# Performance work log

Hardware: AMD Instinct MI355X
Metric: run time of the kernel (lower is better)

The kernel has to match this reference:

```python
import jax, jax.numpy as jnp
import numpy as np

V, D, S, H, L, BATCH = 32000, 1024, 1024, 16, 8, 2
HD = D // H  # head_size = 64


def _pyramid_mask(block_size):
    # Faithful to the torch buffer construction of 'pyr' for BIDIRECTIONAL mode.
    h = block_size // 2
    tril = np.tril(np.ones((h, h), dtype=np.float32))
    top = np.repeat(np.flip(tril, axis=1), 2, axis=0)            # (block_size, h)
    reps = np.array([2] * (h - 1) + [1])
    bot = np.concatenate([np.zeros((1, h), dtype=np.float32),
                          np.repeat(tril, reps, axis=0)], axis=0)  # (block_size, h)
    return np.concatenate([top, bot], axis=1)                     # (block_size, block_size)


def _layernorm(x, g, b, eps=1e-5):
    mu = jnp.mean(x, axis=-1, keepdims=True)
    var = jnp.mean((x - mu) ** 2, axis=-1, keepdims=True)
    return (x - mu) * jax.lax.rsqrt(var + eps) * g + b


def setup_inputs() -> dict:
    key = jax.random.key(0)
    ks = jax.random.split(key, 12)
    sd = 0.02
    inp = {
        "idx": jax.random.randint(ks[0], (BATCH, S), 0, V),
        "tok_emb": jax.random.normal(ks[1], (V, D), jnp.float32) * sd,
        "pos_emb": jax.random.normal(ks[2], (S, D), jnp.float32) * sd,
        "ln1_g": jnp.ones((L, D), jnp.float32),
        "ln1_b": jnp.zeros((L, D), jnp.float32),
        "wq": jax.random.normal(ks[3], (L, D, D), jnp.float32) * sd,
        "wk": jax.random.normal(ks[4], (L, D, D), jnp.float32) * sd,
        "wv": jax.random.normal(ks[5], (L, D, D), jnp.float32) * sd,
        "wproj": jax.random.normal(ks[6], (L, D, D), jnp.float32) * sd,
        "bproj": jnp.zeros((L, D), jnp.float32),
        "ln2_g": jnp.ones((L, D), jnp.float32),
        "ln2_b": jnp.zeros((L, D), jnp.float32),
        "w1": jax.random.normal(ks[7], (L, D, 4 * D), jnp.float32) * sd,
        "b1": jnp.zeros((L, 4 * D), jnp.float32),
        "w2": jax.random.normal(ks[8], (L, 4 * D, D), jnp.float32) * sd,
        "b2": jnp.zeros((L, D), jnp.float32),
        "lnf_g": jnp.ones((D,), jnp.float32),
        "lnf_b": jnp.zeros((D,), jnp.float32),
        "wlm": jax.random.normal(ks[9], (D, 2 * V), jnp.float32) * sd,
        "blm": jnp.zeros((2 * V,), jnp.float32),
    }
    return inp


def reference(idx, tok_emb, pos_emb, ln1_g, ln1_b, wq, wk, wv, wproj, bproj,
              ln2_g, ln2_b, w1, b1, w2, b2, lnf_g, lnf_b, wlm, blm):
    B, T = idx.shape
    # pyr[:T, (S-T)//2 : S - (S-T)//2]; with T == S this is the full mask.
    pyr = jnp.asarray(_pyramid_mask(S))
    lo = (S - T) // 2
    mask = pyr[:T, lo:S - lo] == 0  # True where masked out
    scale = HD ** -0.5

    x = tok_emb[idx] + pos_emb[:T]  # [B, T, D]
    for l in range(L):
        h = _layernorm(x, ln1_g[l], ln1_b[l])
        q = (h @ wq[l]).reshape(B, T, H, HD)
        k = (h @ wk[l]).reshape(B, T, H, HD)
        v = (h @ wv[l]).reshape(B, T, H, HD)
        wei = jnp.einsum('bthd,bshd->bhts', q, k) * scale  # [B, H, T, T]
        wei = jnp.where(mask, -jnp.inf, wei)
        wei = jax.nn.softmax(wei, axis=-1)  # dropout=0 (eval)
        att = jnp.einsum('bhts,bshd->bthd', wei, v).reshape(B, T, D)
        x = x + att @ wproj[l] + bproj[l]
        h2 = _layernorm(x, ln2_g[l], ln2_b[l])
        x = x + jax.nn.relu(h2 @ w1[l] + b1[l]) @ w2[l] + b2[l]
    x = _layernorm(x, lnf_g, lnf_b)
    logits = x @ wlm + blm  # [B, T, 2*V]
    return logits
```

## Files before the change

### kernel.cpp

```cpp
#include <hip/hip_runtime.h>

typedef __attribute__((ext_vector_type(8))) __bf16 bf16x8;
typedef __attribute__((ext_vector_type(4))) float f32x4;
typedef __attribute__((ext_vector_type(4))) unsigned int u32x4;
typedef __attribute__((ext_vector_type(2))) unsigned int u32x2;

__device__ __forceinline__ unsigned short f2bf(float f) {
  unsigned int u = __float_as_uint(f);
  u += 0x7fffu + ((u >> 16) & 1u);
  return (unsigned short)(u >> 16);
}

__device__ __forceinline__ void gload16(const void* g, void* l) {
  __builtin_amdgcn_global_load_lds(
      (const __attribute__((address_space(1))) unsigned int*)g,
      (__attribute__((address_space(3))) unsigned int*)l, 16, 0, 0);
}

__global__ __launch_bounds__(256) void embed_k(const int* __restrict__ idx,
    const float* __restrict__ tok, const float* __restrict__ pos,
    float* __restrict__ x) {
  int row = blockIdx.x;
  int t = row & 1023;
  int c = threadIdx.x << 2;
  int id = idx[row];
  f32x4 a = *(const f32x4*)(tok + ((size_t)id << 10) + c);
  f32x4 p = *(const f32x4*)(pos + ((size_t)t << 10) + c);
  a += p;
  *(f32x4*)(x + ((size_t)row << 10) + c) = a;
}

__global__ __launch_bounds__(256) void ln_k(const float* __restrict__ x,
    const float* __restrict__ g, const float* __restrict__ bta,
    unsigned short* __restrict__ out) {
  __shared__ float red[4];
  int row = blockIdx.x, tid = threadIdx.x;
  const float* xr = x + ((size_t)row << 10);
  f32x4 xv = *(const f32x4*)(xr + (tid << 2));
  float s = xv[0] + xv[1] + xv[2] + xv[3];
  #pragma unroll
  for (int off = 32; off; off >>= 1) s += __shfl_xor(s, off);
  if ((tid & 63) == 0) red[tid >> 6] = s;
  __syncthreads();
  float mean = (red[0] + red[1] + red[2] + red[3]) * (1.f / 1024.f);
  __syncthreads();
  f32x4 d = xv - mean;
  float s2 = d[0]*d[0] + d[1]*d[1] + d[2]*d[2] + d[3]*d[3];
  #pragma unroll
  for (int off = 32; off; off >>= 1) s2 += __shfl_xor(s2, off);
  if ((tid & 63) == 0) red[tid >> 6] = s2;
  __syncthreads();
  float var = (red[0] + red[1] + red[2] + red[3]) * (1.f / 1024.f);
  float rs = rsqrtf(var + 1e-5f);
  f32x4 gv = *(const f32x4*)(g + (tid << 2));
  f32x4 bv = *(const f32x4*)(bta + (tid << 2));
  unsigned int p0 = (unsigned int)f2bf(d[0]*rs*gv[0] + bv[0]) |
                    ((unsigned int)f2bf(d[1]*rs*gv[1] + bv[1]) << 16);
  unsigned int p1 = (unsigned int)f2bf(d[2]*rs*gv[2] + bv[2]) |
                    ((unsigned int)f2bf(d[3]*rs*gv[3] + bv[3]) << 16);
  u32x2 o; o[0] = p0; o[1] = p1;
  *(u32x2*)(out + ((size_t)row << 10) + (tid << 2)) = o;
}

__global__ __launch_bounds__(256) void transp_k(const float* __restrict__ in,
    unsigned short* __restrict__ out, int R, int C) {
  __shared__ unsigned short tile[64 * 65];
  size_t lay = (size_t)blockIdx.z * R * C;
  int c0 = blockIdx.x << 6, r0 = blockIdx.y << 6;
  int t = threadIdx.x;
  #pragma unroll
  for (int i = 0; i < 4; i++) {
    int e = (i << 10) + (t << 2);
    int r = e >> 6, c = e & 63;
    f32x4 v = *(const f32x4*)(in + lay + (size_t)(r0 + r) * C + c0 + c);
    tile[r * 65 + c]     = f2bf(v[0]);
    tile[r * 65 + c + 1] = f2bf(v[1]);
    tile[r * 65 + c + 2] = f2bf(v[2]);
    tile[r * 65 + c + 3] = f2bf(v[3]);
  }
  __syncthreads();
  #pragma unroll
  for (int i = 0; i < 4; i++) {
    int e = (i << 10) + (t << 2);
    int cc = e >> 6, rr = e & 63;
    unsigned int a0 = tile[(rr + 0) * 65 + cc];
    unsigned int a1 = tile[(rr + 1) * 65 + cc];
    unsigned int a2 = tile[(rr + 2) * 65 + cc];
    unsigned int a3 = tile[(rr + 3) * 65 + cc];
    u32x2 pk; pk[0] = a0 | (a1 << 16); pk[1] = a2 | (a3 << 16);
    *(u32x2*)(out + lay + (size_t)(c0 + cc) * R + r0 + rr) = pk;
  }
}

#define VMC6 asm volatile("s_waitcnt vmcnt(6)" ::: "memory")
#define VMC8 asm volatile("s_waitcnt vmcnt(8)" ::: "memory")
#define VMC2 asm volatile("s_waitcnt vmcnt(2)" ::: "memory")
#define VMC0 asm volatile("s_waitcnt vmcnt(0)" ::: "memory")

__global__ __launch_bounds__(512, 2) void gemm256_k(
    const unsigned short* __restrict__ A, const unsigned short* __restrict__ Bt,
    const float* __restrict__ bias, float* __restrict__ o32,
    unsigned short* __restrict__ obf, int M, int N, int K, int relu) {
  __shared__ unsigned short lds[2][2][2][8192];
  int mb = M >> 8;
  int wg = blockIdx.x, nwg = gridDim.x;
  int cpx = nwg >> 3;
  int swz = (wg & 7) * cpx + (wg >> 3);
  int bm = swz % mb, bn = swz / mb;
  int m0 = bm << 8, n0 = bn << 8;
  int tid = threadIdx.x, lane = tid & 63, wave = tid >> 6;
  int wrow = wave >> 2, wcol = wave & 3;
  int lrow = lane & 15, g4 = lane >> 4, l7 = lane & 7;
  f32x4 acc[8][4] = {};
  bf16x8 af[8], bfv[4];
  const unsigned short* Ag = A + (size_t)m0 * K;
  const unsigned short* Bg = Bt + (size_t)n0 * K;
  auto stage = [&](int op, int b, int h, int kt) {
    const unsigned short* gb = (op ? Bg : Ag) + ((size_t)(h << 7)) * K + kt;
    char* lb = (char*)&lds[op][b][h][0];
    #pragma unroll
    for (int g = 0; g < 2; g++) {
      int row = (g << 6) + (wave << 3) + (lane >> 3);
      int klog = ((lane & 7) ^ ((lane >> 3) & 7)) << 3;
      gload16(gb + (size_t)row * K + klog, lb + (g << 13) + (wave << 10));
    }
  };

#define PH(bi, qa, qb, LA, LB, STG, VM)                                        \
  {                                                                            \
    if (LA) {                                                                  \
      const unsigned short* Ah = &lds[0][bi][qa][0];                           \
      _Pragma("unroll")                                                        \
      for (int i = 0; i < 4; i++) {                                            \
        int rl = (wrow << 6) + (i << 4) + lrow;                                \
        af[i*2+0] = *(const bf16x8*)(Ah + rl * 64 + ((g4 ^ l7) << 3));         \
        af[i*2+1] = *(const bf16x8*)(Ah + rl * 64 + (((4 + g4) ^ l7) << 3));   \
      }                                                                        \
    }                                                                          \
    if (LB) {                                                                  \
      const unsigned short* Bh = &lds[1][bi][qb][0];                           \
      _Pragma("unroll")                                                        \
      for (int j = 0; j < 2; j++) {                                            \
        int cl = (wcol << 5) + (j << 4) + lrow;                                \
        bfv[j*2+0] = *(const bf16x8*)(Bh + cl * 64 + ((g4 ^ l7) << 3));        \
        bfv[j*2+1] = *(const bf16x8*)(Bh + cl * 64 + (((4 + g4) ^ l7) << 3));  \
      }                                                                        \
    }                                                                          \
    STG;                                                                       \
    __builtin_amdgcn_s_barrier();                                              \
    asm volatile("s_waitcnt lgkmcnt(0)" ::: "memory");                         \
    __builtin_amdgcn_sched_barrier(0);                                         \
    __builtin_amdgcn_s_setprio(1);                                             \
    _Pragma("unroll")                                                          \
    for (int i = 0; i < 4; i++)                                                \
      _Pragma("unroll")                                                        \
      for (int j = 0; j < 2; j++) {                                            \
        acc[(qa)*4+i][(qb)*2+j] = __builtin_amdgcn_mfma_f32_16x16x32_bf16(     \
            af[i*2+0], bfv[j*2+0], acc[(qa)*4+i][(qb)*2+j], 0, 0, 0);          \
        acc[(qa)*4+i][(qb)*2+j] = __builtin_amdgcn_mfma_f32_16x16x32_bf16(     \
            af[i*2+1], bfv[j*2+1], acc[(qa)*4+i][(qb)*2+j], 0, 0, 0);          \
      }                                                                        \
    __builtin_amdgcn_s_setprio(0);                                             \
    VM;                                                                        \
    __builtin_amdgcn_s_barrier();                                              \
  }

  int nt = K >> 6;
  int nit = nt >> 1;
  stage(0, 0, 0, 0); stage(1, 0, 0, 0); stage(1, 0, 1, 0); stage(0, 0, 1, 0);
  stage(0, 1, 0, 64);
  VMC2;
  __builtin_amdgcn_s_barrier();
  for (int it = 0; it < nit; ++it) {
    int kT1 = ((it << 1) + 1) << 6;
    int kT2 = ((it << 1) + 2) << 6;
    int kT3 = ((it << 1) + 3) << 6;
    bool m2 = (it + 1) < nit;
    PH(0, 0, 0, 1, 1, { stage(1, 1, 1, kT1); stage(1, 1, 0, kT1); }, )
    PH(0, 0, 1, 0, 1, { stage(0, 1, 1, kT1); }, )
    PH(0, 1, 1, 1, 0, if (m2) { stage(0, 0, 0, kT2); }, )
    PH(0, 1, 0, 0, 1, if (m2) { stage(1, 0, 1, kT2); },
       if (m2) { VMC6; } else { VMC2; })
    PH(1, 0, 0, 1, 1, if (m2) { stage(1, 0, 0, kT2); }, )
    PH(1, 0, 1, 0, 1, if (m2) { stage(0, 0, 1, kT2); },
       if (m2) { VMC8; } else { VMC0; })
    PH(1, 1, 1, 1, 0, if (m2) { stage(0, 1, 0, kT3); }, )
    PH(1, 1, 0, 0, 1, , if (m2) { VMC2; })
  }
#undef PH
  int frow = g4 << 2;
  #pragma unroll
  for (int rt = 0; rt < 8; rt++) {
    int qa = rt >> 2, i = rt & 3;
    int grow = m0 + (qa << 7) + (wrow << 6) + (i << 4) + frow;
    #pragma unroll
    for (int ct = 0; ct < 4; ct++) {
      int qb = ct >> 1, j = ct & 1;
      int gcol = n0 + (qb << 7) + (wcol << 5) + (j << 4) + lrow;
      float bb = bias ? bias[gcol] : 0.f;
      f32x4 av = acc[rt][ct];
      #pragma unroll
      for (int r = 0; r < 4; r++) {
        float vv = av[r] + bb;
        if (relu) vv = fmaxf(vv, 0.f);
        if (o32) o32[(size_t)(grow + r) * N + gcol] = vv;
        else obf[(size_t)(grow + r) * N + gcol] = f2bf(vv);
      }
    }
  }
}

__global__ __launch_bounds__(256) void gemm_bt(
    const unsigned short* __restrict__ A,
    const unsigned short* __restrict__ Bt0, const unsigned short* __restrict__ Bt1,
    const unsigned short* __restrict__ Bt2,
    const float* __restrict__ bias, const float* resid,
    unsigned short* __restrict__ ob0, unsigned short* __restrict__ ob1,
    unsigned short* __restrict__ vtout, float* o32,
    int M, int N, int K, int relu) {
  __shared__ unsigned short As[128 * 64];
  __shared__ unsigned short Bs[128 * 64];
  int nbp = N >> 7;
  int which = blockIdx.x / nbp;
  int bx = blockIdx.x - which * nbp;
  const unsigned short* Bt = which == 0 ? Bt0 : (which == 1 ? Bt1 : Bt2);
  int m0 = blockIdx.y << 7, n0 = bx << 7;
  int tid = threadIdx.x, lane = tid & 63, wave = tid >> 6;
  int wr = (wave >> 1) << 6, wc = (wave & 1) << 6;
  int lrow = lane & 15, lk8 = (lane >> 4) << 3;
  int wbase = wave << 12;
  f32x4 acc[4][4] = {};
  const unsigned short* Ag = A + (size_t)m0 * K;
  const unsigned short* Bg = Bt + (size_t)n0 * K;
  for (int k0 = 0; k0 < K; k0 += 64) {
    #pragma unroll
    for (int i = 0; i < 4; i++) {
      int o = wbase + (i << 10) + (lane << 4);
      int r = o >> 7, c = (o & 127) >> 1;
      gload16(Ag + (size_t)r * K + k0 + c, (char*)As + wbase + (i << 10));
      gload16(Bg + (size_t)r * K + k0 + c, (char*)Bs + wbase + (i << 10));
    }
    __syncthreads();
    #pragma unroll
    for (int ks = 0; ks < 2; ks++) {
      bf16x8 af[4], bfv[4];
      #pragma unroll
      for (int i = 0; i < 4; i++)
        af[i] = *(const bf16x8*)(As + ((wr + (i << 4) + lrow) << 6) + (ks << 5) + lk8);
      #pragma unroll
      for (int i = 0; i < 4; i++)
        bfv[i] = *(const bf16x8*)(Bs + ((wc + (i << 4) + lrow) << 6) + (ks << 5) + lk8);
      #pragma unroll
      for (int mi = 0; mi < 4; mi++)
        #pragma unroll
        for (int ni = 0; ni < 4; ni++)
          acc[mi][ni] = __builtin_amdgcn_mfma_f32_16x16x32_bf16(af[mi], bfv[ni], acc[mi][ni], 0, 0, 0);
    }
    __syncthreads();
  }
  int fr = (lane >> 4) << 2;
  #pragma unroll
  for (int mi = 0; mi < 4; mi++) {
    #pragma unroll
    for (int ni = 0; ni < 4; ni++) {
      int row = m0 + wr + (mi << 4) + fr;
      int col = n0 + wc + (ni << 4) + lrow;
      f32x4 av = acc[mi][ni];
      if (bias) {
        float bb = bias[col];
        av[0] += bb; av[1] += bb; av[2] += bb; av[3] += bb;
      }
      if (relu) {
        av[0] = fmaxf(av[0], 0.f); av[1] = fmaxf(av[1], 0.f);
        av[2] = fmaxf(av[2], 0.f); av[3] = fmaxf(av[3], 0.f);
      }
      if (which == 2) {
        u32x2 pk;
        pk[0] = (unsigned int)f2bf(av[0]) | ((unsigned int)f2bf(av[1]) << 16);
        pk[1] = (unsigned int)f2bf(av[2]) | ((unsigned int)f2bf(av[3]) << 16);
        *(u32x2*)(vtout + (((size_t)(row >> 10) * 16 + (col >> 6)) * 64 + (col & 63)) * 1024
                  + (row & 1023)) = pk;
      } else if (o32) {
        #pragma unroll
        for (int r = 0; r < 4; r++) {
          size_t off = (size_t)(row + r) * N + col;
          float vvv = av[r];
          if (resid) vvv += resid[off];
          o32[off] = vvv;
        }
      } else {
        unsigned short* ob = which == 0 ? ob0 : ob1;
        #pragma unroll
        for (int r = 0; r < 4; r++)
          ob[(size_t)(row + r) * N + col] = f2bf(av[r]);
      }
    }
  }
}

__global__ __launch_bounds__(256) void gemm_splitk(
    const unsigned short* __restrict__ A, const unsigned short* __restrict__ Bt,
    float* __restrict__ pbuf, int M, int N, int K, int KS) {
  __shared__ unsigned short As[128 * 64];
  __shared__ unsigned short Bs[128 * 64];
  int m0 = blockIdx.y << 7, n0 = blockIdx.x << 7;
  int kz = blockIdx.z * KS;
  int tid = threadIdx.x, lane = tid & 63, wave = tid >> 6;
  int wr = (wave >> 1) << 6, wc = (wave & 1) << 6;
  int lrow = lane & 15, lk8 = (lane >> 4) << 3;
  int wbase = wave << 12;
  f32x4 acc[4][4] = {};
  const unsigned short* Ag = A + (size_t)m0 * K;
  const unsigned short* Bg = Bt + (size_t)n0 * K;
  for (int k0 = kz; k0 < kz + KS; k0 += 64) {
    #pragma unroll
    for (int i = 0; i < 4; i++) {
      int o = wbase + (i << 10) + (lane << 4);
      int r = o >> 7, c = (o & 127) >> 1;
      gload16(Ag + (size_t)r * K + k0 + c, (char*)As + wbase + (i << 10));
      gload16(Bg + (size_t)r * K + k0 + c, (char*)Bs + wbase + (i << 10));
    }
    __syncthreads();
    #pragma unroll
    for (int ks = 0; ks < 2; ks++) {
      bf16x8 af[4], bfv[4];
      #pragma unroll
      for (int i = 0; i < 4; i++)
        af[i] = *(const bf16x8*)(As + ((wr + (i << 4) + lrow) << 6) + (ks << 5) + lk8);
      #pragma unroll
      for (int i = 0; i < 4; i++)
        bfv[i] = *(const bf16x8*)(Bs + ((wc + (i << 4) + lrow) << 6) + (ks << 5) + lk8);
      #pragma unroll
      for (int mi = 0; mi < 4; mi++)
        #pragma unroll
        for (int ni = 0; ni < 4; ni++)
          acc[mi][ni] = __builtin_amdgcn_mfma_f32_16x16x32_bf16(af[mi], bfv[ni], acc[mi][ni], 0, 0, 0);
    }
    __syncthreads();
  }
  int fr = (lane >> 4) << 2;
  float* pb = pbuf + (size_t)blockIdx.z * M * N;
  #pragma unroll
  for (int mi = 0; mi < 4; mi++)
    #pragma unroll
    for (int ni = 0; ni < 4; ni++) {
      int row = m0 + wr + (mi << 4) + fr;
      int col = n0 + wc + (ni << 4) + lrow;
      #pragma unroll
      for (int r = 0; r < 4; r++)
        pb[(size_t)(row + r) * N + col] = acc[mi][ni][r];
    }
}

__global__ __launch_bounds__(256) void reduce_k(float* __restrict__ x,
    const float* __restrict__ pbuf, const float* __restrict__ bias, int nz) {
  int row = blockIdx.x, c = threadIdx.x << 2;
  size_t off = ((size_t)row << 10) + c;
  f32x4 s = *(const f32x4*)(bias + c);
  for (int z = 0; z < nz; z++)
    s += *(const f32x4*)(pbuf + ((size_t)z << 21) + off);
  f32x4 xv = *(const f32x4*)(x + off);
  xv += s;
  *(f32x4*)(x + off) = xv;
}

__global__ __launch_bounds__(256) void attn64_k(
    const unsigned short* __restrict__ q, const unsigned short* __restrict__ k,
    const unsigned short* __restrict__ vt, unsigned short* __restrict__ att) {
  __shared__ unsigned short Ks[64 * 72];
  __shared__ unsigned short Vs[64 * 72];
  __shared__ unsigned short Ps[4][16 * 72];
  int t0 = blockIdx.x << 6;
  int h = blockIdx.y, b = blockIdx.z;
  int tid = threadIdx.x, lane = tid & 63, w = tid >> 6;
  int lrow = lane & 15, lk8 = (lane >> 4) << 3, fr = (lane >> 4) << 2;
  int qrow = t0 + (w << 4) + lrow;
  size_t qoff = ((size_t)((b << 10) + qrow) << 10) + (h << 6);
  bf16x8 a0 = *(const bf16x8*)(q + qoff + lk8);
  bf16x8 a1 = *(const bf16x8*)(q + qoff + 32 + lk8);
  float m_[4] = {-1e30f, -1e30f, -1e30f, -1e30f};
  float l_[4] = {0.f, 0.f, 0.f, 0.f};
  f32x4 o_[4] = {};
  int s_lo = (511 - ((t0 + 63) >> 1)) & ~63;
  int s_hi = 511 + ((t0 + 64) >> 1);
  int s_end = (s_hi + 64) & ~63;
  int krow = tid >> 2, kc = (tid & 3) << 4;
  size_t vbase = ((size_t)((b << 4) + h) << 16) + ((size_t)krow << 10);
  unsigned short* Psw = &Ps[w][0];
  for (int s0 = s_lo; s0 < s_end; s0 += 64) {
    size_t koff = (((size_t)((b << 10) + s0 + krow)) << 10) + (h << 6) + kc;
    u32x4 kv0 = *(const u32x4*)(k + koff);
    u32x4 kv1 = *(const u32x4*)(k + koff + 8);
    u32x4 vv0 = *(const u32x4*)(vt + vbase + s0 + kc);
    u32x4 vv1 = *(const u32x4*)(vt + vbase + s0 + kc + 8);
    *(u32x4*)(Ks + krow * 72 + kc) = kv0;
    *(u32x4*)(Ks + krow * 72 + kc + 8) = kv1;
    *(u32x4*)(Vs + krow * 72 + kc) = vv0;
    *(u32x4*)(Vs + krow * 72 + kc + 8) = vv1;
    __syncthreads();
    f32x4 sc[4];
    #pragma unroll
    for (int sb = 0; sb < 4; sb++) {
      f32x4 z = {};
      bf16x8 kb0 = *(const bf16x8*)(Ks + ((sb << 4) + lrow) * 72 + lk8);
      bf16x8 kb1 = *(const bf16x8*)(Ks + ((sb << 4) + lrow) * 72 + 32 + lk8);
      z = __builtin_amdgcn_mfma_f32_16x16x32_bf16(a0, kb0, z, 0, 0, 0);
      z = __builtin_amdgcn_mfma_f32_16x16x32_bf16(a1, kb1, z, 0, 0, 0);
      sc[sb] = z;
    }
    #pragma unroll
    for (int r = 0; r < 4; r++) {
      int t = t0 + (w << 4) + fr + r;
      int lov = 511 - (t >> 1), hiv = 511 + ((t + 1) >> 1);
      float px[4];
      float tm = -1e30f;
      #pragma unroll
      for (int sb = 0; sb < 4; sb++) {
        int sX = s0 + (sb << 4) + lrow;
        bool vX = (sX >= lov) && (sX <= hiv);
        float x = vX ? sc[sb][r] * 0.125f : -1e30f;
        px[sb] = x;
        tm = fmaxf(tm, x);
      }
      #pragma unroll
      for (int off = 8; off; off >>= 1) tm = fmaxf(tm, __shfl_xor(tm, off));
      float nm = fmaxf(m_[r], tm);
      float sca = __expf(m_[r] - nm);
      m_[r] = nm;
      float ps = 0.f;
      #pragma unroll
      for (int sb = 0; sb < 4; sb++) {
        float pv = __expf(px[sb] - nm);
        ps += pv;
        Psw[(fr + r) * 72 + (sb << 4) + lrow] = f2bf(pv);
      }
      #pragma unroll
      for (int off = 8; off; off >>= 1) ps += __shfl_xor(ps, off);
      l_[r] = l_[r] * sca + ps;
      #pragma unroll
      for (int nb = 0; nb < 4; nb++) o_[nb][r] *= sca;
    }
    bf16x8 pa0 = *(const bf16x8*)(Psw + lrow * 72 + lk8);
    bf16x8 pa1 = *(const bf16x8*)(Psw + lrow * 72 + 32 + lk8);
    #pragma unroll
    for (int nb = 0; nb < 4; nb++) {
      bf16x8 vb0 = *(const bf16x8*)(Vs + ((nb << 4) + lrow) * 72 + lk8);
      bf16x8 vb1 = *(const bf16x8*)(Vs + ((nb << 4) + lrow) * 72 + 32 + lk8);
      o_[nb] = __builtin_amdgcn_mfma_f32_16x16x32_bf16(pa0, vb0, o_[nb], 0, 0, 0);
      o_[nb] = __builtin_amdgcn_mfma_f32_16x16x32_bf16(pa1, vb1, o_[nb], 0, 0, 0);
    }
    __syncthreads();
  }
  #pragma unroll
  for (int nb = 0; nb < 4; nb++)
    #pragma unroll
    for (int r = 0; r < 4; r++) {
      float ov = o_[nb][r] / l_[r];
      att[((size_t)((b << 10) + t0 + (w << 4) + fr + r) << 10) + (h << 6) + (nb << 4) + lrow]
          = f2bf(ov);
    }
}

extern "C" void kernel_launch(void* const* d_in, const int* in_sizes, int n_in,
                              void* d_out, int out_size, void* d_ws, size_t ws_size,
                              hipStream_t stream) {
  (void)in_sizes; (void)n_in; (void)out_size;
  const int*   idx  = (const int*)d_in[0];
  const float* tok  = (const float*)d_in[1];
  const float* pos  = (const float*)d_in[2];
  const float* ln1g = (const float*)d_in[3];
  const float* ln1b = (const float*)d_in[4];
  const float* wq   = (const float*)d_in[5];
  const float* wk   = (const float*)d_in[6];
  const float* wv   = (const float*)d_in[7];
  const float* wpj  = (const float*)d_in[8];
  const float* bpj  = (const float*)d_in[9];
  const float* ln2g = (const float*)d_in[10];
  const float* ln2b = (const float*)d_in[11];
  const float* w1   = (const float*)d_in[12];
  const float* b1   = (const float*)d_in[13];
  const float* w2   = (const float*)d_in[14];
  const float* b2   = (const float*)d_in[15];
  const float* lnfg = (const float*)d_in[16];
  const float* lnfb = (const float*)d_in[17];
  const float* wlm  = (const float*)d_in[18];
  const float* blm  = (const float*)d_in[19];
  float* out = (float*)d_out;

  char* ws = (char*)d_ws;
  const size_t MB = 1u << 20;
  float*          x    = (float*)ws;
  unsigned short* hb   = (unsigned short*)(ws + 8 * MB);
  unsigned short* qb   = (unsigned short*)(ws + 12 * MB);
  unsigned short* kb   = (unsigned short*)(ws + 16 * MB);
  unsigned short* vbuf = (unsigned short*)(ws + 20 * MB);
  unsigned short* ab   = (unsigned short*)(ws + 24 * MB);
  unsigned short* m1   = (unsigned short*)(ws + 28 * MB);
  const int M = 2048, D = 1024;

  int nz; float* pb;
  if (ws_size >= 408 * MB) { nz = 4; pb = (float*)(ws + 376 * MB); }
  else                     { nz = 2; pb = (float*)(ws + 8 * MB); }

  embed_k<<<dim3(2048), dim3(256), 0, stream>>>(idx, tok, pos, x);

  unsigned short* wqT  = (unsigned short*)(ws + 44 * MB);
  unsigned short* wkT  = (unsigned short*)(ws + 60 * MB);
  unsigned short* wvT  = (unsigned short*)(ws + 76 * MB);
  unsigned short* wpT  = (unsigned short*)(ws + 92 * MB);
  unsigned short* w1T  = (unsigned short*)(ws + 108 * MB);
  unsigned short* w2T  = (unsigned short*)(ws + 172 * MB);
  unsigned short* wlmT = (unsigned short*)(ws + 236 * MB);
  transp_k<<<dim3(16, 16, 8), 256, 0, stream>>>(wq,   wqT,  1024, 1024);
  transp_k<<<dim3(16, 16, 8), 256, 0, stream>>>(wk,   wkT,  1024, 1024);
  transp_k<<<dim3(16, 16, 8), 256, 0, stream>>>(wv,   wvT,  1024, 1024);
  transp_k<<<dim3(16, 16, 8), 256, 0, stream>>>(wpj,  wpT,  1024, 1024);
  transp_k<<<dim3(64, 16, 8), 256, 0, stream>>>(w1,   w1T,  1024, 4096);
  transp_k<<<dim3(16, 64, 8), 256, 0, stream>>>(w2,   w2T,  4096, 1024);
  transp_k<<<dim3(1000, 16, 1), 256, 0, stream>>>(wlm, wlmT, 1024, 64000);
  for (int l = 0; l < 8; l++) {
    size_t wo = (size_t)l << 20;
    ln_k<<<2048, 256, 0, stream>>>(x, ln1g + l*D, ln1b + l*D, hb);
    gemm_bt<<<dim3(24, 16), 256, 0, stream>>>(hb, wqT + wo, wkT + wo, wvT + wo,
        nullptr, nullptr, qb, kb, vbuf, nullptr, M, D, D, 0);
    attn64_k<<<dim3(16, 16, 2), 256, 0, stream>>>(qb, kb, vbuf, ab);
    gemm_bt<<<dim3(8, 16), 256, 0, stream>>>(ab, wpT + wo, nullptr, nullptr,
        bpj + l*D, x, nullptr, nullptr, nullptr, x, M, D, D, 0);
    ln_k<<<2048, 256, 0, stream>>>(x, ln2g + l*D, ln2b + l*D, hb);
    gemm_bt<<<dim3(32, 16), 256, 0, stream>>>(hb, w1T + ((size_t)l << 22), nullptr, nullptr,
        b1 + (size_t)l*4*D, nullptr, m1, nullptr, nullptr, nullptr, M, 4*D, D, 1);
    gemm_splitk<<<dim3(8, 16, nz), 256, 0, stream>>>(m1, w2T + ((size_t)l << 22),
        pb, M, D, 4*D, 4*D / nz);
    reduce_k<<<2048, 256, 0, stream>>>(x, pb, b2 + l*D, nz);
  }
  ln_k<<<2048, 256, 0, stream>>>(x, lnfg, lnfb, hb);
  gemm256_k<<<dim3(2000), 512, 0, stream>>>(hb, wlmT,
      blm, out, nullptr, M, 64000, D, 0);
}
```

Measured before the change: 2.175 ms.

## Halve GEMM K-tile to 32 to shrink LDS and raise occupancy

The 256x256 GEMM kernel now stages K-slices of 32 instead of 64. This halves the LDS buffers and the A/B fragment registers, and launch bounds now ask for 4 workgroups per CU instead of 2. The LDS swizzle, the per-thread load mapping and the vmcnt wait counts are rederived for one 16-byte load per stage. The trade-off is twice as many loop iterations and barriers per K, with less MFMA work between each synchronisation.

```diff
diff --git a/kernel.cpp b/kernel.cpp
--- a/kernel.cpp
+++ b/kernel.cpp
@@ -92,16 +92,16 @@
   }
 }
 
-#define VMC6 asm volatile("s_waitcnt vmcnt(6)" ::: "memory")
-#define VMC8 asm volatile("s_waitcnt vmcnt(8)" ::: "memory")
-#define VMC2 asm volatile("s_waitcnt vmcnt(2)" ::: "memory")
+#define VMC4 asm volatile("s_waitcnt vmcnt(4)" ::: "memory")
+#define VMC3 asm volatile("s_waitcnt vmcnt(3)" ::: "memory")
+#define VMC1 asm volatile("s_waitcnt vmcnt(1)" ::: "memory")
 #define VMC0 asm volatile("s_waitcnt vmcnt(0)" ::: "memory")
 
-__global__ __launch_bounds__(512, 2) void gemm256_k(
+__global__ __launch_bounds__(512, 4) void gemm256_k(
     const unsigned short* __restrict__ A, const unsigned short* __restrict__ Bt,
     const float* __restrict__ bias, float* __restrict__ o32,
     unsigned short* __restrict__ obf, int M, int N, int K, int relu) {
-  __shared__ unsigned short lds[2][2][2][8192];
+  __shared__ unsigned short lds[2][2][2][4096];
   int mb = M >> 8;
   int wg = blockIdx.x, nwg = gridDim.x;
   int cpx = nwg >> 3;
@@ -110,20 +110,18 @@
   int m0 = bm << 8, n0 = bn << 8;
   int tid = threadIdx.x, lane = tid & 63, wave = tid >> 6;
   int wrow = wave >> 2, wcol = wave & 3;
-  int lrow = lane & 15, g4 = lane >> 4, l7 = lane & 7;
+  int lrow = lane & 15, g4 = lane >> 4;
+  int sw = (g4 ^ ((lrow >> 1) & 3)) << 3;
   f32x4 acc[8][4] = {};
-  bf16x8 af[8], bfv[4];
+  bf16x8 af[4], bfv[2];
   const unsigned short* Ag = A + (size_t)m0 * K;
   const unsigned short* Bg = Bt + (size_t)n0 * K;
   auto stage = [&](int op, int b, int h, int kt) {
     const unsigned short* gb = (op ? Bg : Ag) + ((size_t)(h << 7)) * K + kt;
     char* lb = (char*)&lds[op][b][h][0];
-    #pragma unroll
-    for (int g = 0; g < 2; g++) {
-      int row = (g << 6) + (wave << 3) + (lane >> 3);
-      int klog = ((lane & 7) ^ ((lane >> 3) & 7)) << 3;
-      gload16(gb + (size_t)row * K + klog, lb + (g << 13) + (wave << 10));
-    }
+    int row = tid >> 2;
+    int grp = (tid & 3) ^ ((tid >> 3) & 3);
+    gload16(gb + (size_t)row * K + (grp << 3), lb + (wave << 10));
   };
 
 #define PH(bi, qa, qb, LA, LB, STG, VM)                                        \
@@ -133,8 +131,7 @@
       _Pragma("unroll")                                                        \
       for (int i = 0; i < 4; i++) {                                            \
         int rl = (wrow << 6) + (i << 4) + lrow;                                \
-        af[i*2+0] = *(const bf16x8*)(Ah + rl * 64 + ((g4 ^ l7) << 3));         \
-        af[i*2+1] = *(const bf16x8*)(Ah + rl * 64 + (((4 + g4) ^ l7) << 3));   \
+        af[i] = *(const bf16x8*)(Ah + rl * 32 + sw);                           \
       }                                                                        \
     }                                                                          \
     if (LB) {                                                                  \
@@ -142,8 +139,7 @@
       _Pragma("unroll")                                                        \
       for (int j = 0; j < 2; j++) {                                            \
         int cl = (wcol << 5) + (j << 4) + lrow;                                \
-        bfv[j*2+0] = *(const bf16x8*)(Bh + cl * 64 + ((g4 ^ l7) << 3));        \
-        bfv[j*2+1] = *(const bf16x8*)(Bh + cl * 64 + (((4 + g4) ^ l7) << 3));  \
+        bfv[j] = *(const bf16x8*)(Bh + cl * 32 + sw);                          \
       }                                                                        \
     }                                                                          \
     STG;                                                                       \
@@ -154,38 +150,34 @@
     _Pragma("unroll")                                                          \
     for (int i = 0; i < 4; i++)                                                \
       _Pragma("unroll")                                                        \
-      for (int j = 0; j < 2; j++) {                                            \
+      for (int j = 0; j < 2; j++)                                              \
         acc[(qa)*4+i][(qb)*2+j] = __builtin_amdgcn_mfma_f32_16x16x32_bf16(     \
-            af[i*2+0], bfv[j*2+0], acc[(qa)*4+i][(qb)*2+j], 0, 0, 0);          \
-        acc[(qa)*4+i][(qb)*2+j] = __builtin_amdgcn_mfma_f32_16x16x32_bf16(     \
-            af[i*2+1], bfv[j*2+1], acc[(qa)*4+i][(qb)*2+j], 0, 0, 0);          \
-      }                                                                        \
+            af[i], bfv[j], acc[(qa)*4+i][(qb)*2+j], 0, 0, 0);                  \
     __builtin_amdgcn_s_setprio(0);                                             \
     VM;                                                                        \
     __builtin_amdgcn_s_barrier();                                              \
   }
 
-  int nt = K >> 6;
-  int nit = nt >> 1;
+  int nit = K >> 6;
   stage(0, 0, 0, 0); stage(1, 0, 0, 0); stage(1, 0, 1, 0); stage(0, 0, 1, 0);
-  stage(0, 1, 0, 64);
-  VMC2;
+  stage(0, 1, 0, 32);
+  VMC1;
   __builtin_amdgcn_s_barrier();
   for (int it = 0; it < nit; ++it) {
-    int kT1 = ((it << 1) + 1) << 6;
-    int kT2 = ((it << 1) + 2) << 6;
-    int kT3 = ((it << 1) + 3) << 6;
+    int kT1 = ((it << 1) + 1) << 5;
+    int kT2 = ((it << 1) + 2) << 5;
+    int kT3 = ((it << 1) + 3) << 5;
     bool m2 = (it + 1) < nit;
     PH(0, 0, 0, 1, 1, { stage(1, 1, 1, kT1); stage(1, 1, 0, kT1); }, )
     PH(0, 0, 1, 0, 1, { stage(0, 1, 1, kT1); }, )
     PH(0, 1, 1, 1, 0, if (m2) { stage(0, 0, 0, kT2); }, )
     PH(0, 1, 0, 0, 1, if (m2) { stage(1, 0, 1, kT2); },
-       if (m2) { VMC6; } else { VMC2; })
+       if (m2) { VMC3; } else { VMC1; })
     PH(1, 0, 0, 1, 1, if (m2) { stage(1, 0, 0, kT2); }, )
     PH(1, 0, 1, 0, 1, if (m2) { stage(0, 0, 1, kT2); },
-       if (m2) { VMC8; } else { VMC0; })
+       if (m2) { VMC4; } else { VMC0; })
     PH(1, 1, 1, 1, 0, if (m2) { stage(0, 1, 0, kT3); }, )
-    PH(1, 1, 0, 0, 1, , if (m2) { VMC2; })
+    PH(1, 1, 0, 0, 1, , if (m2) { VMC1; })
   }
 #undef PH
   int frow = g4 << 2;
```

New measurement: 3.990 ms. 83.4% more time.
